# Optimization experiments

Measured on AMD Instinct MI355X. Metric: run time of the kernel, lower is better.

## Reference

```python
import jax, jax.numpy as jnp
import numpy as np

B = 4_194_304  # batch size


def setup_inputs() -> dict:
    key = jax.random.key(0)
    k1, k2, k3, k4 = jax.random.split(key, 4)
    X = jax.random.normal(k1, (B, 4), dtype=jnp.float32)
    mu = jax.random.normal(k2, (B, 2), dtype=jnp.float32)
    sigma = jax.random.uniform(k3, (B,), dtype=jnp.float32)
    u = jax.random.normal(k4, (B, 2), dtype=jnp.float32)
    Q = jnp.array([[1.0, 0.0, 0.0, 0.0],
                   [0.0, 1.0, 0.0, 0.0],
                   [0.0, 0.0, 0.5, 0.0],
                   [0.0, 0.0, 0.0, 0.5]], dtype=jnp.float32)
    R = jnp.array([[0.1, 0.0], [0.0, 0.1]], dtype=jnp.float32)
    x_target = jnp.array([1.0, 0.0, 0.0, 0.0], dtype=jnp.float32)
    return {"X": X, "mu": mu, "sigma": sigma, "u": u,
            "Q": Q, "R": R, "x_target": x_target}


def reference(X, mu, sigma, u, Q, R, x_target):
    omega = 0.6
    # Hard-coded system matrices from HJBModel.__init__
    f = jnp.array([[0.0, 0.0, 1.0, 0.0],
                   [0.0, 0.0, 0.0, 1.0],
                   [0.0, omega, 0.0, 0.0],
                   [-omega, 0.0, 0.0, 0.0]], dtype=X.dtype)
    G = jnp.array([[0.3, 0.0], [0.0, 0.25], [1.0, 0.0], [0.0, 1.0]], dtype=X.dtype)
    COV = jnp.array([[0.0, 0.0], [0.0, 0.0], [0.5, 0.0], [0.0, 0.5]], dtype=X.dtype)

    xr = X - x_target                                    # [B,4]
    # V = xr^T Q xr
    V = jnp.einsum('bi,ij,bj->b', xr, Q, xr)             # [B]
    # dyn = f X + G u + COV mu
    dyn = X @ f.T + u @ G.T + mu @ COV.T                 # [B,4]
    # grad1 @ dyn = 2 xr^T Q dyn
    g1dyn = 2.0 * jnp.einsum('bi,ij,bj->b', xr, Q, dyn)  # [B]
    # 0.5 u^T R u
    uRu = 0.5 * jnp.einsum('bi,ij,bj->b', u, R, u)       # [B]
    # trace term: 0.5 sigma^2 * trace(2Q @ COV COV^T)
    tr_const = jnp.trace((2.0 * Q) @ (COV @ COV.T))      # scalar
    trace_term = 0.5 * sigma ** 2 * tr_const             # [B]
    return jnp.mean(g1dyn + V + uRu + trace_term)
```

## Files before the change

### kernel.cpp

```cpp
#include <hip/hip_runtime.h>

#define BLOCK 256
#define GRID  1024

__device__ __forceinline__ float row_val(
    float x0, float x1, float x2, float x3,
    float u0, float u1, float m0, float m1, float sg,
    const float* q, float r0, float r1, float r2, float r3,
    float t0, float t1, float t2, float t3, float tr_c)
{
    float xr0 = x0 - t0, xr1 = x1 - t1, xr2 = x2 - t2, xr3 = x3 - t3;
    float dyn0 = x2 + 0.3f * u0;
    float dyn1 = x3 + 0.25f * u1;
    float dyn2 = 0.6f * x1 + u0 + 0.5f * m0;
    float dyn3 = -0.6f * x0 + u1 + 0.5f * m1;
    float qx0 = xr0 * q[0] + xr1 * q[4] + xr2 * q[8]  + xr3 * q[12];
    float qx1 = xr0 * q[1] + xr1 * q[5] + xr2 * q[9]  + xr3 * q[13];
    float qx2 = xr0 * q[2] + xr1 * q[6] + xr2 * q[10] + xr3 * q[14];
    float qx3 = xr0 * q[3] + xr1 * q[7] + xr2 * q[11] + xr3 * q[15];
    float V    = qx0 * xr0 + qx1 * xr1 + qx2 * xr2 + qx3 * xr3;
    float g1   = 2.0f * (qx0 * dyn0 + qx1 * dyn1 + qx2 * dyn2 + qx3 * dyn3);
    float uRu  = 0.5f * (u0 * (r0 * u0 + r1 * u1) + u1 * (r2 * u0 + r3 * u1));
    float tt   = 0.5f * sg * sg * tr_c;
    return V + g1 + uRu + tt;
}

__global__ __launch_bounds__(BLOCK) void hjb_loss_kernel(
    const float* __restrict__ X,
    const float* __restrict__ mu,
    const float* __restrict__ sigma,
    const float* __restrict__ u,
    const float* __restrict__ Q,
    const float* __restrict__ R,
    const float* __restrict__ xt,
    float* __restrict__ out,
    int nquads, float inv_B)
{
    float q[16];
#pragma unroll
    for (int i = 0; i < 16; ++i) q[i] = Q[i];
    const float r0 = R[0], r1 = R[1], r2 = R[2], r3 = R[3];
    const float t0 = xt[0], t1 = xt[1], t2 = xt[2], t3 = xt[3];
    const float tr_c = 0.5f * (q[10] + q[15]);

    const float4* __restrict__ X4  = reinterpret_cast<const float4*>(X);
    const float4* __restrict__ u4  = reinterpret_cast<const float4*>(u);
    const float4* __restrict__ mu4 = reinterpret_cast<const float4*>(mu);
    const float4* __restrict__ s4  = reinterpret_cast<const float4*>(sigma);

    float acc = 0.0f;
    const int tid    = blockIdx.x * BLOCK + threadIdx.x;
    const int stride = gridDim.x * BLOCK;

    for (int qd = tid; qd < nquads; qd += stride) {
        float4 xa = X4[qd * 4 + 0];
        float4 xb = X4[qd * 4 + 1];
        float4 xc = X4[qd * 4 + 2];
        float4 xd = X4[qd * 4 + 3];
        float4 ua = u4[qd * 2 + 0];
        float4 ub = u4[qd * 2 + 1];
        float4 ma = mu4[qd * 2 + 0];
        float4 mb = mu4[qd * 2 + 1];
        float4 sg = s4[qd];

        acc += row_val(xa.x, xa.y, xa.z, xa.w, ua.x, ua.y, ma.x, ma.y, sg.x,
                       q, r0, r1, r2, r3, t0, t1, t2, t3, tr_c);
        acc += row_val(xb.x, xb.y, xb.z, xb.w, ua.z, ua.w, ma.z, ma.w, sg.y,
                       q, r0, r1, r2, r3, t0, t1, t2, t3, tr_c);
        acc += row_val(xc.x, xc.y, xc.z, xc.w, ub.x, ub.y, mb.x, mb.y, sg.z,
                       q, r0, r1, r2, r3, t0, t1, t2, t3, tr_c);
        acc += row_val(xd.x, xd.y, xd.z, xd.w, ub.z, ub.w, mb.z, mb.w, sg.w,
                       q, r0, r1, r2, r3, t0, t1, t2, t3, tr_c);
    }

    acc *= inv_B;

#pragma unroll
    for (int off = 32; off > 0; off >>= 1)
        acc += __shfl_down(acc, off, 64);

    __shared__ float wave_sums[BLOCK / 64];
    const int lane = threadIdx.x & 63;
    const int wid  = threadIdx.x >> 6;
    if (lane == 0) wave_sums[wid] = acc;
    __syncthreads();

    if (wid == 0) {
        float v = (lane < BLOCK / 64) ? wave_sums[lane] : 0.0f;
        v += __shfl_down(v, 2, 64);
        v += __shfl_down(v, 1, 64);
        if (lane == 0) atomicAdd(out, v);
    }
}

extern "C" void kernel_launch(void* const* d_in, const int* in_sizes, int n_in,
                              void* d_out, int out_size, void* d_ws, size_t ws_size,
                              hipStream_t stream) {
    const float* X     = (const float*)d_in[0];
    const float* mu    = (const float*)d_in[1];
    const float* sigma = (const float*)d_in[2];
    const float* u     = (const float*)d_in[3];
    const float* Q     = (const float*)d_in[4];
    const float* R     = (const float*)d_in[5];
    const float* xt    = (const float*)d_in[6];
    float* out = (float*)d_out;

    const int B = in_sizes[2];
    const int nquads = B / 4;
    const float inv_B = 1.0f / (float)B;

    hipMemsetAsync(out, 0, sizeof(float) * out_size, stream);
    hjb_loss_kernel<<<GRID, BLOCK, 0, stream>>>(
        X, mu, sigma, u, Q, R, xt, out, nquads, inv_B);
}
```

Measured before the change: 170.4 us.

## Switch to row-per-thread coalesced loads and enlarge grid

Each thread now processes one row per step, with a stride of the whole grid, and keeps four independent rows in flight per iteration. Loads become float4 for X, float2 for u and mu, and scalar for sigma, so adjacent lanes read adjacent rows. Before, each thread read a 64-byte chunk of X and made strided 16-byte loads across lanes. The grid grows from 1024 to 4096 blocks to raise the number of outstanding memory requests. In exchange, the u, mu and sigma loads are narrower, the tail needs a remainder loop, and four times as many block atomics hit the output.

```diff
diff --git a/kernel.cpp b/kernel.cpp
--- a/kernel.cpp
+++ b/kernel.cpp
@@ -1,7 +1,7 @@
 #include <hip/hip_runtime.h>
 
 #define BLOCK 256
-#define GRID  1024
+#define GRID  4096
 
 __device__ __forceinline__ float row_val(
     float x0, float x1, float x2, float x3,
@@ -34,7 +34,7 @@
     const float* __restrict__ R,
     const float* __restrict__ xt,
     float* __restrict__ out,
-    int nquads, float inv_B)
+    int B, float inv_B)
 {
     float q[16];
 #pragma unroll
@@ -43,33 +43,41 @@
     const float t0 = xt[0], t1 = xt[1], t2 = xt[2], t3 = xt[3];
     const float tr_c = 0.5f * (q[10] + q[15]);
 
-    const float4* __restrict__ X4  = reinterpret_cast<const float4*>(X);
-    const float4* __restrict__ u4  = reinterpret_cast<const float4*>(u);
-    const float4* __restrict__ mu4 = reinterpret_cast<const float4*>(mu);
-    const float4* __restrict__ s4  = reinterpret_cast<const float4*>(sigma);
+    const float4*  __restrict__ X4  = reinterpret_cast<const float4*>(X);
+    const float2*  __restrict__ u2  = reinterpret_cast<const float2*>(u);
+    const float2*  __restrict__ mu2 = reinterpret_cast<const float2*>(mu);
 
     float acc = 0.0f;
-    const int tid    = blockIdx.x * BLOCK + threadIdx.x;
-    const int stride = gridDim.x * BLOCK;
+    const int tid = blockIdx.x * BLOCK + threadIdx.x;
+    const int T   = gridDim.x * BLOCK;
 
-    for (int qd = tid; qd < nquads; qd += stride) {
-        float4 xa = X4[qd * 4 + 0];
-        float4 xb = X4[qd * 4 + 1];
-        float4 xc = X4[qd * 4 + 2];
-        float4 xd = X4[qd * 4 + 3];
-        float4 ua = u4[qd * 2 + 0];
-        float4 ub = u4[qd * 2 + 1];
-        float4 ma = mu4[qd * 2 + 0];
-        float4 mb = mu4[qd * 2 + 1];
-        float4 sg = s4[qd];
+    int r = tid;
+    for (; r + 3 * T < B; r += 4 * T) {
+        const int ra = r, rb = r + T, rc = r + 2 * T, rd = r + 3 * T;
+        float4 xa = X4[ra];  float4 xb = X4[rb];
+        float4 xc = X4[rc];  float4 xd = X4[rd];
+        float2 ua = u2[ra];  float2 ub = u2[rb];
+        float2 uc = u2[rc];  float2 ud = u2[rd];
+        float2 ma = mu2[ra]; float2 mb = mu2[rb];
+        float2 mc = mu2[rc]; float2 md = mu2[rd];
+        float  sa = sigma[ra]; float sb = sigma[rb];
+        float  sc = sigma[rc]; float sd = sigma[rd];
 
-        acc += row_val(xa.x, xa.y, xa.z, xa.w, ua.x, ua.y, ma.x, ma.y, sg.x,
+        acc += row_val(xa.x, xa.y, xa.z, xa.w, ua.x, ua.y, ma.x, ma.y, sa,
                        q, r0, r1, r2, r3, t0, t1, t2, t3, tr_c);
-        acc += row_val(xb.x, xb.y, xb.z, xb.w, ua.z, ua.w, ma.z, ma.w, sg.y,
+        acc += row_val(xb.x, xb.y, xb.z, xb.w, ub.x, ub.y, mb.x, mb.y, sb,
                        q, r0, r1, r2, r3, t0, t1, t2, t3, tr_c);
-        acc += row_val(xc.x, xc.y, xc.z, xc.w, ub.x, ub.y, mb.x, mb.y, sg.z,
+        acc += row_val(xc.x, xc.y, xc.z, xc.w, uc.x, uc.y, mc.x, mc.y, sc,
                        q, r0, r1, r2, r3, t0, t1, t2, t3, tr_c);
-        acc += row_val(xd.x, xd.y, xd.z, xd.w, ub.z, ub.w, mb.z, mb.w, sg.w,
+        acc += row_val(xd.x, xd.y, xd.z, xd.w, ud.x, ud.y, md.x, md.y, sd,
+                       q, r0, r1, r2, r3, t0, t1, t2, t3, tr_c);
+    }
+    for (; r < B; r += T) {
+        float4 x = X4[r];
+        float2 uu = u2[r];
+        float2 mm = mu2[r];
+        float  sg = sigma[r];
+        acc += row_val(x.x, x.y, x.z, x.w, uu.x, uu.y, mm.x, mm.y, sg,
                        q, r0, r1, r2, r3, t0, t1, t2, t3, tr_c);
     }
 
@@ -106,10 +114,9 @@
     float* out = (float*)d_out;
 
     const int B = in_sizes[2];
-    const int nquads = B / 4;
     const float inv_B = 1.0f / (float)B;
 
     hipMemsetAsync(out, 0, sizeof(float) * out_size, stream);
     hjb_loss_kernel<<<GRID, BLOCK, 0, stream>>>(
-        X, mu, sigma, u, Q, R, xt, out, nquads, inv_B);
+        X, mu, sigma, u, Q, R, xt, out, B, inv_B);
 }
```

New measurement: 183.8 us. +7.9%, slower.
